# Kernel tuning notes

Measured on AMD Instinct MI355X. Metric: run time of the kernel, lower is better.

The kernel has to match this reference:

```python
import jax, jax.numpy as jnp
import numpy as np

N = 50000      # nodes
E = 800000     # edges (before self-loops)
D = 128        # hid_d
H = 8          # heads
C = D // H     # per-head channels
L = 3          # layers
SLOPE = 0.2    # GATv2 leaky_relu negative slope
EPS = 1e-5     # LayerNorm eps


def setup_inputs() -> dict:
    key = jax.random.key(0)
    ks = jax.random.split(key, 8)
    x = jax.random.normal(ks[0], (N, D), dtype=jnp.float32)
    ei = jax.random.randint(ks[1], (2, E), 0, N, dtype=jnp.int32)
    s = 1.0 / np.sqrt(D)
    Wl = jax.random.normal(ks[2], (L, D, D), dtype=jnp.float32) * s   # source transform per layer
    Wr = jax.random.normal(ks[3], (L, D, D), dtype=jnp.float32) * s   # target transform per layer
    att = jax.random.normal(ks[4], (L, H, C), dtype=jnp.float32) * (1.0 / np.sqrt(C))
    bias = jnp.zeros((L, D), dtype=jnp.float32)
    gamma = jnp.ones((L, D), dtype=jnp.float32)
    beta = jnp.zeros((L, D), dtype=jnp.float32)
    return {"x": x, "Wl": Wl, "Wr": Wr, "att": att, "bias": bias,
            "gamma": gamma, "beta": beta, "ei": ei}


def _layernorm(y, g, b):
    mu = jnp.mean(y, axis=-1, keepdims=True)
    var = jnp.mean(jnp.square(y - mu), axis=-1, keepdims=True)
    return (y - mu) * jax.lax.rsqrt(var + EPS) * g + b


def reference(x, Wl, Wr, att, bias, gamma, beta, ei):
    # append self-loops (PyG GATv2Conv default add_self_loops=True)
    loops = jnp.arange(N, dtype=ei.dtype)
    src = jnp.concatenate([ei[0], loops])  # [E+N]
    dst = jnp.concatenate([ei[1], loops])  # [E+N]
    h = x
    for l in range(L):
        xl = (h @ Wl[l]).reshape(N, H, C)   # source-side features
        xr = (h @ Wr[l]).reshape(N, H, C)   # target-side features
        feat = xl[src] + xr[dst]            # [E+N, H, C] per-edge gather
        logits = jnp.einsum('ehc,hc->eh', jax.nn.leaky_relu(feat, SLOPE), att[l])
        # segment softmax over incoming edges of each dst node
        m = jax.ops.segment_max(logits, dst, num_segments=N)
        ex = jnp.exp(logits - m[dst])
        denom = jax.ops.segment_sum(ex, dst, num_segments=N)
        alpha = ex / denom[dst]             # [E+N, H]
        msg = alpha[:, :, None] * xl[src]   # [E+N, H, C]
        out = jax.ops.segment_sum(msg, dst, num_segments=N).reshape(N, H * C) + bias[l]
        # wrapper: h = h + dropout(elu(norm(gat(h)))) ; dropout = identity (eval)
        h = h + jax.nn.elu(_layernorm(out, gamma[l], beta[l]))
    return h
```

## Files before the change

### kernel.cpp

```cpp
#include <hip/hip_runtime.h>
#include <hip/hip_fp16.h>
#include <math.h>

#define N_NODES 50000
#define N_EDGES 800000
#define D 128
#define L 3
#define SLOPE 0.2f
#define LN_EPS 1e-5f
#define ETOT (N_EDGES + N_NODES)
#define SCAN_BLOCKS ((N_NODES + 1023) / 1024)

typedef _Float16 half8 __attribute__((ext_vector_type(8)));
typedef _Float16 h4v  __attribute__((ext_vector_type(4)));
typedef _Float16 h2v  __attribute__((ext_vector_type(2)));
typedef float f32x4 __attribute__((ext_vector_type(4)));


__global__ void rank_hist_kernel(const int* __restrict__ ei, int* __restrict__ counts,
                                 int* __restrict__ rank) {
    int idx = blockIdx.x * blockDim.x + threadIdx.x;
    if (idx >= ETOT) return;
    int d = (idx < N_EDGES) ? ei[N_EDGES + idx] : (idx - N_EDGES);
    rank[idx] = atomicAdd(&counts[d], 1);
}

__global__ __launch_bounds__(1024) void scan1_kernel(const int* __restrict__ counts,
                                                     int* __restrict__ offsets,
                                                     int* __restrict__ bsum) {
    __shared__ int wsum[16];
    int tid = threadIdx.x;
    int lane = tid & 63, w = tid >> 6;
    int i = blockIdx.x * 1024 + tid;
    int v = (i < N_NODES) ? counts[i] : 0;
    int sc = v;
    #pragma unroll
    for (int off = 1; off < 64; off <<= 1) {
        int u = __shfl_up(sc, off);
        if (lane >= off) sc += u;
    }
    if (lane == 63) wsum[w] = sc;
    __syncthreads();
    if (w == 0) {
        int t2 = (lane < 16) ? wsum[lane] : 0;
        #pragma unroll
        for (int off = 1; off < 16; off <<= 1) {
            int u = __shfl_up(t2, off);
            if (lane >= off) t2 += u;
        }
        if (lane < 16) wsum[lane] = t2;
    }
    __syncthreads();
    int wpref = (w == 0) ? 0 : wsum[w - 1];
    if (i < N_NODES) offsets[i] = wpref + sc - v;
    if (tid == 0) bsum[blockIdx.x] = wsum[15];
}

__global__ __launch_bounds__(64) void scan2_kernel(const int* __restrict__ bsum,
                                                   int* __restrict__ bpre) {
    int lane = threadIdx.x;
    int v = (lane < SCAN_BLOCKS) ? bsum[lane] : 0;
    int sc = v;
    #pragma unroll
    for (int off = 1; off < 64; off <<= 1) {
        int u = __shfl_up(sc, off);
        if (lane >= off) sc += u;
    }
    if (lane < SCAN_BLOCKS) bpre[lane] = sc - v;
}

__global__ __launch_bounds__(1024) void scan3_kernel(int* __restrict__ offsets,
                                                     const int* __restrict__ bpre) {
    int i = blockIdx.x * 1024 + threadIdx.x;
    if (i < N_NODES) offsets[i] += bpre[blockIdx.x];
    if (i == 0) offsets[N_NODES] = ETOT;
}

__global__ void scatter_kernel(const int* __restrict__ ei, const int* __restrict__ offsets,
                               const int* __restrict__ rank,
                               unsigned short* __restrict__ sorted16) {
    int idx = blockIdx.x * blockDim.x + threadIdx.x;
    if (idx >= ETOT) return;
    int s, d;
    if (idx < N_EDGES) { s = ei[idx]; d = ei[N_EDGES + idx]; }
    else               { s = d = idx - N_EDGES; }
    sorted16[offsets[d] + rank[idx]] = (unsigned short)s;
}


__global__ __launch_bounds__(1024) void deg_hist_kernel(const int* __restrict__ counts,
                                                        int* __restrict__ blockhist) {
    __shared__ int lh[256];
    int tid = threadIdx.x;
    if (tid < 256) lh[tid] = 0;
    __syncthreads();
    int i = blockIdx.x * 1024 + tid;
    if (i < N_NODES) {
        int d = counts[i]; if (d > 255) d = 255;
        atomicAdd(&lh[d], 1);
    }
    __syncthreads();
    if (tid < 256) blockhist[blockIdx.x * 256 + tid] = lh[tid];
}

__global__ __launch_bounds__(256) void deg_scan_kernel(int* __restrict__ blockhist) {
    int d = threadIdx.x;
    int run = 0;
    #pragma unroll 1
    for (int b = 0; b < SCAN_BLOCKS; ++b) {
        int c = blockhist[b * 256 + d];
        blockhist[b * 256 + d] = run;
        run += c;
    }
    __shared__ int wsum[4];
    int lane = d & 63, w = d >> 6;
    int sc = run;
    #pragma unroll
    for (int off = 1; off < 64; off <<= 1) {
        int u = __shfl_up(sc, off);
        if (lane >= off) sc += u;
    }
    if (lane == 63) wsum[w] = sc;
    __syncthreads();
    int wpre = 0;
    #pragma unroll
    for (int k = 0; k < 4; ++k) wpre += (k < w) ? wsum[k] : 0;
    int binbase = wpre + sc - run;
    #pragma unroll 1
    for (int b = 0; b < SCAN_BLOCKS; ++b)
        blockhist[b * 256 + d] += binbase;
}

__global__ __launch_bounds__(1024) void deg_scatter_kernel(const int* __restrict__ counts,
                                                           const int* __restrict__ blockhist,
                                                           int* __restrict__ perm) {
    __shared__ int lh[256];
    int tid = threadIdx.x;
    if (tid < 256) lh[tid] = 0;
    __syncthreads();
    int i = blockIdx.x * 1024 + tid;
    if (i >= N_NODES) return;
    int d = counts[i]; if (d > 255) d = 255;
    int r = atomicAdd(&lh[d], 1);
    int pos = blockhist[blockIdx.x * 256 + d] + r;
    perm[pos] = i;
}


__global__ __launch_bounds__(256) void wfrag_kernel(const float* __restrict__ Wl,
                                                    const float* __restrict__ Wr,
                                                    _Float16* __restrict__ Wfrag) {
    int u = blockIdx.x * 256 + threadIdx.x;
    if (u >= 3 * 4096) return;
    int lane = u & 63, nt = (u >> 6) & 7, kt = (u >> 9) & 3, y = (u >> 11) & 1, l = u >> 12;
    int r = lane & 15, q = lane >> 4;
    const float* W = (y ? Wr : Wl) + (size_t)l * D * D;
    half8 v;
    #pragma unroll
    for (int j = 0; j < 8; ++j)
        v[j] = (_Float16)W[(kt * 32 + q * 8 + j) * D + nt * 16 + r];
    *(half8*)&Wfrag[(size_t)u * 8] = v;
}


template<bool AHALF>
__global__ __launch_bounds__(256) void gemm_mfma_kernel(
        const void* __restrict__ hsrc, const _Float16* __restrict__ WfragL,
        _Float16* __restrict__ xlh, _Float16* __restrict__ xrh) {
    __shared__ half8 Afrag[1024];
    int t = threadIdx.x;
    int row0 = blockIdx.x * 64;
    int w = t >> 6, lane = t & 63;
    int y = w >> 1, nh = w & 1;

    half8 bfrag[16];
    #pragma unroll
    for (int kt = 0; kt < 4; ++kt)
        #pragma unroll
        for (int n = 0; n < 4; ++n) {
            int nt = nh * 4 + n;
            bfrag[kt * 4 + n] =
                *(const half8*)&WfragL[(size_t)(((y * 4 + kt) * 8 + nt) * 64 + lane) * 8];
        }

    {
        int kt = t >> 6, q = (t >> 4) & 3, r = t & 15;
        int kc = kt * 4 + q;
        #pragma unroll
        for (int i = 0; i < 4; ++i) {
            int row = row0 + i * 16 + r;
            half8 v = {};
            if (row < N_NODES) {
                if constexpr (AHALF) {
                    const _Float16* h16 = (const _Float16*)hsrc;
                    v = *(const half8*)&h16[(size_t)row * D + kc * 8];
                } else {
                    const float* p = &((const float*)hsrc)[(size_t)row * D + kc * 8];
                    float4 f0 = *(const float4*)p;
                    float4 f1 = *(const float4*)(p + 4);
                    v[0] = (_Float16)f0.x; v[1] = (_Float16)f0.y;
                    v[2] = (_Float16)f0.z; v[3] = (_Float16)f0.w;
                    v[4] = (_Float16)f1.x; v[5] = (_Float16)f1.y;
                    v[6] = (_Float16)f1.z; v[7] = (_Float16)f1.w;
                }
            }
            Afrag[i * 256 + t] = v;
        }
    }
    __syncthreads();

    f32x4 acc[16];
    #pragma unroll
    for (int i = 0; i < 16; ++i) acc[i] = (f32x4){0.f, 0.f, 0.f, 0.f};
    #pragma unroll
    for (int mt = 0; mt < 4; ++mt) {
        #pragma unroll
        for (int kt = 0; kt < 4; ++kt) {
            half8 a = Afrag[mt * 256 + kt * 64 + lane];
            #pragma unroll
            for (int n = 0; n < 4; ++n)
                acc[mt * 4 + n] = __builtin_amdgcn_mfma_f32_16x16x32_f16(
                    a, bfrag[kt * 4 + n], acc[mt * 4 + n], 0, 0, 0);
        }
    }

    _Float16* out = y ? xrh : xlh;
    int rq = lane >> 4, rc = lane & 15;
    #pragma unroll
    for (int mt = 0; mt < 4; ++mt) {
        int rbase = row0 + mt * 16 + rq * 4;
        #pragma unroll
        for (int n = 0; n < 4; ++n) {
            int nt = nh * 4 + n;
            #pragma unroll
            for (int reg = 0; reg < 4; ++reg) {
                int row = rbase + reg;
                if (row < N_NODES)
                    out[(size_t)row * D + nt * 16 + rc] = (_Float16)acc[mt * 4 + n][reg];
            }
        }
    }
}


__device__ __forceinline__ float pair_reduce2(float p) {
    int t;
    t = __builtin_amdgcn_update_dpp(0, __float_as_int(p), 0xB1, 0xF, 0xF, true);
    p += __int_as_float(t);
    return p;
}

__device__ __forceinline__ float logit8(half8 v, half8 xr, const h2v* att4, h2v slope2) {
    float p = 0.f;
    #pragma unroll
    for (int i = 0; i < 4; ++i) {
        h2v a; a[0] = v[2 * i];  a[1] = v[2 * i + 1];
        h2v b; b[0] = xr[2 * i]; b[1] = xr[2 * i + 1];
        h2v f  = a + b;
        h2v lf = __builtin_elementwise_max(f, f * slope2);
        p = __builtin_amdgcn_fdot2(lf, att4[i], p, false);
    }
    return p;
}

template<int KUN, bool MASK>
__device__ __forceinline__ void edge_block(
        int j, int idx_bp, unsigned off, unsigned laneoff, const char* xlb,
        half8 xr8, const h2v* att4, h2v slope2, int cnt,
        float& s, float* acc) {
    half8 vs[KUN];
    #pragma unroll
    for (int k = 0; k < KUN; ++k) {
        int o = __builtin_amdgcn_ds_bpermute(idx_bp + 4 * (j + k), (int)off);
        vs[k] = *(const half8*)(xlb + ((unsigned)o + laneoff));
    }
    #pragma unroll
    for (int k = 0; k < KUN; ++k) {
        float p = logit8(vs[k], xr8, att4, slope2);
        p = pair_reduce2(p);
        float e = __builtin_amdgcn_exp2f(p);
        if (MASK) e = (j + k < cnt) ? e : 0.f;
        s += e;
        #pragma unroll
        for (int i = 0; i < 8; ++i)
            acc[i] = fmaf(e, (float)vs[k][i], acc[i]);
    }
}

__global__ __launch_bounds__(256) void gat_node_kernel(
        const _Float16* __restrict__ xlh, const _Float16* __restrict__ xrh,
        const int* __restrict__ offsets, const unsigned short* __restrict__ sorted16,
        const int* __restrict__ perm,
        const float* __restrict__ att_l, const float* __restrict__ bias_l,
        const float* __restrict__ gamma_l, const float* __restrict__ beta_l,
        const float* __restrict__ hin, float* __restrict__ hout,
        _Float16* __restrict__ h16out) {
    int wid = (blockIdx.x * blockDim.x + threadIdx.x) >> 6;
    if (wid * 4 >= N_NODES) return;
    int lane = threadIdx.x & 63;
    int g = lane >> 4, hl = lane & 15;
    int node = perm[wid * 4 + g];
    unsigned laneoff = hl * 16u;
    int idx_bp = g << 6;

    half8 xr8 = *(const half8*)&xrh[(size_t)node * D + hl * 8];
    float4 af0 = *(const float4*)&att_l[hl * 8];
    float4 af1 = *(const float4*)&att_l[hl * 8 + 4];
    h2v att4[4], slope2;
    att4[0][0] = (_Float16)(af0.x * 1.44269504f);
    att4[0][1] = (_Float16)(af0.y * 1.44269504f);
    att4[1][0] = (_Float16)(af0.z * 1.44269504f);
    att4[1][1] = (_Float16)(af0.w * 1.44269504f);
    att4[2][0] = (_Float16)(af1.x * 1.44269504f);
    att4[2][1] = (_Float16)(af1.y * 1.44269504f);
    att4[3][0] = (_Float16)(af1.z * 1.44269504f);
    att4[3][1] = (_Float16)(af1.w * 1.44269504f);
    slope2[0] = (_Float16)SLOPE;
    slope2[1] = (_Float16)SLOPE;

    int beg = offsets[node], end = offsets[node + 1];
    int deg = end - beg;
    int d0 = __builtin_amdgcn_readlane(deg, 0);
    int d1 = __builtin_amdgcn_readlane(deg, 16);
    int d2 = __builtin_amdgcn_readlane(deg, 32);
    int d3 = __builtin_amdgcn_readlane(deg, 48);
    int m01 = d0 > d1 ? d0 : d1, m23 = d2 > d3 ? d2 : d3;
    int degMax = m01 > m23 ? m01 : m23;
    int n01 = d0 < d1 ? d0 : d1, n23 = d2 < d3 ? d2 : d3;
    int degMin = n01 < n23 ? n01 : n23;

    float s = 0.f;
    float acc[8] = {0.f, 0.f, 0.f, 0.f, 0.f, 0.f, 0.f, 0.f};
    const char* xlb = (const char*)xlh;

    for (int c0 = 0; c0 < degMax; c0 += 16) {
        int rem = deg - c0;
        int cnt = rem > 16 ? 16 : rem;
        int cl  = cnt > 0 ? (hl < cnt ? hl : cnt - 1) : 0;
        int pos = cnt > 0 ? beg + c0 + cl : beg;
        unsigned off = ((unsigned)sorted16[pos]) << 8;
        int jmax = degMax - c0; if (jmax > 16) jmax = 16;
        int nfull = degMin - c0; if (nfull > 16) nfull = 16; if (nfull < 0) nfull = 0;
        int j = 0;
        for (; j + 8 <= nfull; j += 8)
            edge_block<8, false>(j, idx_bp, off, laneoff, xlb, xr8, att4, slope2,
                                 cnt, s, acc);
        for (; j + 4 <= nfull; j += 4)
            edge_block<4, false>(j, idx_bp, off, laneoff, xlb, xr8, att4, slope2,
                                 cnt, s, acc);
        for (; j + 4 <= jmax; j += 4)
            edge_block<4, true>(j, idx_bp, off, laneoff, xlb, xr8, att4, slope2,
                                cnt, s, acc);
        for (; j < jmax; ++j)
            edge_block<1, true>(j, idx_bp, off, laneoff, xlb, xr8, att4, slope2,
                                cnt, s, acc);
    }

    float inv = 1.f / s;
    float4 b0 = *(const float4*)&bias_l[hl * 8];
    float4 b1 = *(const float4*)&bias_l[hl * 8 + 4];
    float o[8];
    o[0] = acc[0] * inv + b0.x; o[1] = acc[1] * inv + b0.y;
    o[2] = acc[2] * inv + b0.z; o[3] = acc[3] * inv + b0.w;
    o[4] = acc[4] * inv + b1.x; o[5] = acc[5] * inv + b1.y;
    o[6] = acc[6] * inv + b1.z; o[7] = acc[7] * inv + b1.w;
    float sum = ((o[0] + o[1]) + (o[2] + o[3])) + ((o[4] + o[5]) + (o[6] + o[7]));
    float sq  = ((o[0] * o[0] + o[1] * o[1]) + (o[2] * o[2] + o[3] * o[3]))
              + ((o[4] * o[4] + o[5] * o[5]) + (o[6] * o[6] + o[7] * o[7]));
    #pragma unroll
    for (int msk = 1; msk < 16; msk <<= 1) {
        sum += __shfl_xor(sum, msk);
        sq  += __shfl_xor(sq, msk);
    }
    float mu   = sum * (1.f / 128.f);
    float var  = sq * (1.f / 128.f) - mu * mu;
    float rstd = rsqrtf(var + LN_EPS);
    float4 g0 = *(const float4*)&gamma_l[hl * 8];
    float4 g1 = *(const float4*)&gamma_l[hl * 8 + 4];
    float4 e0 = *(const float4*)&beta_l[hl * 8];
    float4 e1 = *(const float4*)&beta_l[hl * 8 + 4];
    float gam[8] = {g0.x, g0.y, g0.z, g0.w, g1.x, g1.y, g1.z, g1.w};
    float bet[8] = {e0.x, e0.y, e0.z, e0.w, e1.x, e1.y, e1.z, e1.w};
    size_t di = (size_t)node * D + hl * 8;
    float4 h0 = *(const float4*)&hin[di];
    float4 h1 = *(const float4*)&hin[di + 4];
    float hv[8] = {h0.x, h0.y, h0.z, h0.w, h1.x, h1.y, h1.z, h1.w};
    float y[8];
    #pragma unroll
    for (int i = 0; i < 8; ++i) {
        float t = (o[i] - mu) * rstd * gam[i] + bet[i];
        t = t > 0.f ? t : __expf(t) - 1.f;
        y[i] = hv[i] + t;
    }
    float4 w0 = make_float4(y[0], y[1], y[2], y[3]);
    float4 w1 = make_float4(y[4], y[5], y[6], y[7]);
    *(float4*)&hout[di]     = w0;
    *(float4*)&hout[di + 4] = w1;
    half8 h16v;
    #pragma unroll
    for (int i = 0; i < 8; ++i) h16v[i] = (_Float16)y[i];
    *(half8*)&h16out[di] = h16v;
}


extern "C" void kernel_launch(void* const* d_in, const int* in_sizes, int n_in,
                              void* d_out, int out_size, void* d_ws, size_t ws_size,
                              hipStream_t stream) {
    const float* x     = (const float*)d_in[0];
    const float* Wl    = (const float*)d_in[1];
    const float* Wr    = (const float*)d_in[2];
    const float* att   = (const float*)d_in[3];
    const float* bias  = (const float*)d_in[4];
    const float* gamma = (const float*)d_in[5];
    const float* beta  = (const float*)d_in[6];
    const int*   ei    = (const int*)d_in[7];
    float* h = (float*)d_out;

    char* ws = (char*)d_ws;
    _Float16* xlh = (_Float16*)ws;   ws += (size_t)N_NODES * D * sizeof(_Float16);
    _Float16* xrh = (_Float16*)ws;   ws += (size_t)N_NODES * D * sizeof(_Float16);
    _Float16* h16 = (_Float16*)ws;   ws += (size_t)N_NODES * D * sizeof(_Float16);
    _Float16* Wfrag = (_Float16*)ws; ws += (size_t)3 * 4096 * 8 * sizeof(_Float16);
    int* offsets = (int*)ws;         ws += (size_t)(N_NODES + 4) * sizeof(int);
    int* counts  = (int*)ws;         ws += (size_t)N_NODES * sizeof(int);
    int* bsum    = (int*)ws;         ws += 64 * sizeof(int);
    int* bpre    = (int*)ws;         ws += 64 * sizeof(int);
    int* blockhist = (int*)ws;       ws += (size_t)SCAN_BLOCKS * 256 * sizeof(int);
    int* perm    = (int*)ws;         ws += (size_t)N_NODES * sizeof(int);
    int* rank    = (int*)ws;         ws += (size_t)ETOT * sizeof(int);
    unsigned short* sorted16 = (unsigned short*)ws;

    wfrag_kernel<<<48, 256, 0, stream>>>(Wl, Wr, Wfrag);
    (void)hipMemsetAsync(counts, 0, (size_t)N_NODES * sizeof(int), stream);
    rank_hist_kernel<<<(ETOT + 255) / 256, 256, 0, stream>>>(ei, counts, rank);
    scan1_kernel<<<SCAN_BLOCKS, 1024, 0, stream>>>(counts, offsets, bsum);
    scan2_kernel<<<1, 64, 0, stream>>>(bsum, bpre);
    scan3_kernel<<<SCAN_BLOCKS, 1024, 0, stream>>>(offsets, bpre);
    scatter_kernel<<<(ETOT + 255) / 256, 256, 0, stream>>>(ei, offsets, rank, sorted16);
    deg_hist_kernel<<<SCAN_BLOCKS, 1024, 0, stream>>>(counts, blockhist);
    deg_scan_kernel<<<1, 256, 0, stream>>>(blockhist);
    deg_scatter_kernel<<<SCAN_BLOCKS, 1024, 0, stream>>>(counts, blockhist, perm);

    int gat_waves  = (N_NODES + 3) / 4;
    int gat_blocks = (gat_waves * 64 + 255) / 256;
    for (int l = 0; l < L; ++l) {
        const float* hin = (l == 0) ? x : h;
        if (l == 0)
            gemm_mfma_kernel<false><<<(N_NODES + 63) / 64, 256, 0, stream>>>(
                x, Wfrag + (size_t)l * 4096 * 8, xlh, xrh);
        else
            gemm_mfma_kernel<true><<<(N_NODES + 63) / 64, 256, 0, stream>>>(
                h16, Wfrag + (size_t)l * 4096 * 8, xlh, xrh);
        gat_node_kernel<<<gat_blocks, 256, 0, stream>>>(
            xlh, xrh, offsets, sorted16, perm,
            att + (size_t)l * D, bias + (size_t)l * D,
            gamma + (size_t)l * D, beta + (size_t)l * D, hin, h, h16);
    }
}
```

Before: 330.0 us.

## Fuse degree-sort kernels into scan kernels, transpose MFMA output, process high-degree nodes first

```diff
diff --git a/kernel.cpp b/kernel.cpp
--- a/kernel.cpp
+++ b/kernel.cpp
@@ -27,12 +27,20 @@
 
 __global__ __launch_bounds__(1024) void scan1_kernel(const int* __restrict__ counts,
                                                      int* __restrict__ offsets,
-                                                     int* __restrict__ bsum) {
+                                                     int* __restrict__ bsum,
+                                                     int* __restrict__ blockhist) {
     __shared__ int wsum[16];
+    __shared__ int lh[256];
     int tid = threadIdx.x;
+    if (tid < 256) lh[tid] = 0;
+    __syncthreads();
     int lane = tid & 63, w = tid >> 6;
     int i = blockIdx.x * 1024 + tid;
     int v = (i < N_NODES) ? counts[i] : 0;
+    if (i < N_NODES) {
+        int d = v; if (d > 255) d = 255;
+        atomicAdd(&lh[d], 1);
+    }
     int sc = v;
     #pragma unroll
     for (int off = 1; off < 64; off <<= 1) {
@@ -54,25 +62,68 @@
     int wpref = (w == 0) ? 0 : wsum[w - 1];
     if (i < N_NODES) offsets[i] = wpref + sc - v;
     if (tid == 0) bsum[blockIdx.x] = wsum[15];
-}
-
-__global__ __launch_bounds__(64) void scan2_kernel(const int* __restrict__ bsum,
-                                                   int* __restrict__ bpre) {
-    int lane = threadIdx.x;
-    int v = (lane < SCAN_BLOCKS) ? bsum[lane] : 0;
-    int sc = v;
+    __syncthreads();
+    if (tid < 256) blockhist[blockIdx.x * 256 + tid] = lh[tid];
+}
+
+__global__ __launch_bounds__(256) void scan2_kernel(const int* __restrict__ bsum,
+                                                    int* __restrict__ bpre,
+                                                    int* __restrict__ blockhist) {
+    int tid = threadIdx.x;
+    if (tid < 64) {
+        int lane = tid;
+        int v = (lane < SCAN_BLOCKS) ? bsum[lane] : 0;
+        int sc = v;
+        #pragma unroll
+        for (int off = 1; off < 64; off <<= 1) {
+            int u = __shfl_up(sc, off);
+            if (lane >= off) sc += u;
+        }
+        if (lane < SCAN_BLOCKS) bpre[lane] = sc - v;
+    }
+    int d = tid;
+    int run = 0;
+    #pragma unroll 1
+    for (int b = 0; b < SCAN_BLOCKS; ++b) {
+        int c = blockhist[b * 256 + d];
+        blockhist[b * 256 + d] = run;
+        run += c;
+    }
+    __shared__ int wsum[4];
+    int lane = d & 63, w = d >> 6;
+    int sc = run;
     #pragma unroll
     for (int off = 1; off < 64; off <<= 1) {
         int u = __shfl_up(sc, off);
         if (lane >= off) sc += u;
     }
-    if (lane < SCAN_BLOCKS) bpre[lane] = sc - v;
+    if (lane == 63) wsum[w] = sc;
+    __syncthreads();
+    int wpre = 0;
+    #pragma unroll
+    for (int k = 0; k < 4; ++k) wpre += (k < w) ? wsum[k] : 0;
+    int binbase = wpre + sc - run;
+    #pragma unroll 1
+    for (int b = 0; b < SCAN_BLOCKS; ++b)
+        blockhist[b * 256 + d] += binbase;
 }
 
 __global__ __launch_bounds__(1024) void scan3_kernel(int* __restrict__ offsets,
-                                                     const int* __restrict__ bpre) {
-    int i = blockIdx.x * 1024 + threadIdx.x;
-    if (i < N_NODES) offsets[i] += bpre[blockIdx.x];
+                                                     const int* __restrict__ bpre,
+                                                     const int* __restrict__ counts,
+                                                     const int* __restrict__ blockhist,
+                                                     int* __restrict__ perm) {
+    __shared__ int lh[256];
+    int tid = threadIdx.x;
+    if (tid < 256) lh[tid] = 0;
+    __syncthreads();
+    int i = blockIdx.x * 1024 + tid;
+    if (i < N_NODES) {
+        offsets[i] += bpre[blockIdx.x];
+        int d = counts[i]; if (d > 255) d = 255;
+        int r = atomicAdd(&lh[d], 1);
+        perm[blockhist[blockIdx.x * 256 + d] + r] = i;
+    }
     if (i == 0) offsets[N_NODES] = ETOT;
 }
 
@@ -88,65 +139,6 @@
 }
 
 
-__global__ __launch_bounds__(1024) void deg_hist_kernel(const int* __restrict__ counts,
-                                                        int* __restrict__ blockhist) {
-    __shared__ int lh[256];
-    int tid = threadIdx.x;
-    if (tid < 256) lh[tid] = 0;
-    __syncthreads();
-    int i = blockIdx.x * 1024 + tid;
-    if (i < N_NODES) {
-        int d = counts[i]; if (d > 255) d = 255;
-        atomicAdd(&lh[d], 1);
-    }
-    __syncthreads();
-    if (tid < 256) blockhist[blockIdx.x * 256 + tid] = lh[tid];
-}
-
-__global__ __launch_bounds__(256) void deg_scan_kernel(int* __restrict__ blockhist) {
-    int d = threadIdx.x;
-    int run = 0;
-    #pragma unroll 1
-    for (int b = 0; b < SCAN_BLOCKS; ++b) {
-        int c = blockhist[b * 256 + d];
-        blockhist[b * 256 + d] = run;
-        run += c;
-    }
-    __shared__ int wsum[4];
-    int lane = d & 63, w = d >> 6;
-    int sc = run;
-    #pragma unroll
-    for (int off = 1; off < 64; off <<= 1) {
-        int u = __shfl_up(sc, off);
-        if (lane >= off) sc += u;
-    }
-    if (lane == 63) wsum[w] = sc;
-    __syncthreads();
-    int wpre = 0;
-    #pragma unroll
-    for (int k = 0; k < 4; ++k) wpre += (k < w) ? wsum[k] : 0;
-    int binbase = wpre + sc - run;
-    #pragma unroll 1
-    for (int b = 0; b < SCAN_BLOCKS; ++b)
-        blockhist[b * 256 + d] += binbase;
-}
-
-__global__ __launch_bounds__(1024) void deg_scatter_kernel(const int* __restrict__ counts,
-                                                           const int* __restrict__ blockhist,
-                                                           int* __restrict__ perm) {
-    __shared__ int lh[256];
-    int tid = threadIdx.x;
-    if (tid < 256) lh[tid] = 0;
-    __syncthreads();
-    int i = blockIdx.x * 1024 + tid;
-    if (i >= N_NODES) return;
-    int d = counts[i]; if (d > 255) d = 255;
-    int r = atomicAdd(&lh[d], 1);
-    int pos = blockhist[blockIdx.x * 256 + d] + r;
-    perm[pos] = i;
-}
-
-
 __global__ __launch_bounds__(256) void wfrag_kernel(const float* __restrict__ Wl,
                                                     const float* __restrict__ Wr,
                                                     _Float16* __restrict__ Wfrag) {
@@ -177,9 +169,9 @@
     #pragma unroll
     for (int kt = 0; kt < 4; ++kt)
         #pragma unroll
-        for (int n = 0; n < 4; ++n) {
-            int nt = nh * 4 + n;
-            bfrag[kt * 4 + n] =
+        for (int f = 0; f < 4; ++f) {
+            int nt = nh * 4 + f;
+            bfrag[kt * 4 + f] =
                 *(const half8*)&WfragL[(size_t)(((y * 4 + kt) * 8 + nt) * 64 + lane) * 8];
         }
 
@@ -213,30 +205,32 @@
     #pragma unroll
     for (int i = 0; i < 16; ++i) acc[i] = (f32x4){0.f, 0.f, 0.f, 0.f};
     #pragma unroll
-    for (int mt = 0; mt < 4; ++mt) {
+    for (int ntile = 0; ntile < 4; ++ntile) {
         #pragma unroll
         for (int kt = 0; kt < 4; ++kt) {
-            half8 a = Afrag[mt * 256 + kt * 64 + lane];
+            half8 a = Afrag[ntile * 256 + kt * 64 + lane];
             #pragma unroll
-            for (int n = 0; n < 4; ++n)
-                acc[mt * 4 + n] = __builtin_amdgcn_mfma_f32_16x16x32_f16(
-                    a, bfrag[kt * 4 + n], acc[mt * 4 + n], 0, 0, 0);
+            for (int f = 0; f < 4; ++f)
+                acc[f * 4 + ntile] = __builtin_amdgcn_mfma_f32_16x16x32_f16(
+                    bfrag[kt * 4 + f], a, acc[f * 4 + ntile], 0, 0, 0);
         }
     }
 
     _Float16* out = y ? xrh : xlh;
-    int rq = lane >> 4, rc = lane & 15;
-    #pragma unroll
-    for (int mt = 0; mt < 4; ++mt) {
-        int rbase = row0 + mt * 16 + rq * 4;
-        #pragma unroll
-        for (int n = 0; n < 4; ++n) {
-            int nt = nh * 4 + n;
+    int nr = lane & 15, fq = lane >> 4;
+    #pragma unroll
+    for (int ntile = 0; ntile < 4; ++ntile) {
+        int row = row0 + ntile * 16 + nr;
+        if (row < N_NODES) {
             #pragma unroll
-            for (int reg = 0; reg < 4; ++reg) {
-                int row = rbase + reg;
-                if (row < N_NODES)
-                    out[(size_t)row * D + nt * 16 + rc] = (_Float16)acc[mt * 4 + n][reg];
+            for (int f = 0; f < 4; ++f) {
+                int fb = nh * 64 + f * 16 + fq * 4;
+                h4v v4;
+                v4[0] = (_Float16)acc[f * 4 + ntile][0];
+                v4[1] = (_Float16)acc[f * 4 + ntile][1];
+                v4[2] = (_Float16)acc[f * 4 + ntile][2];
+                v4[3] = (_Float16)acc[f * 4 + ntile][3];
+                *(h4v*)&out[(size_t)row * D + fb] = v4;
             }
         }
     }
@@ -299,7 +293,7 @@
     if (wid * 4 >= N_NODES) return;
     int lane = threadIdx.x & 63;
     int g = lane >> 4, hl = lane & 15;
-    int node = perm[wid * 4 + g];
+    int node = perm[N_NODES - 4 - wid * 4 + g];
     unsigned laneoff = hl * 16u;
     int idx_bp = g << 6;
 
@@ -433,13 +427,10 @@
     wfrag_kernel<<<48, 256, 0, stream>>>(Wl, Wr, Wfrag);
     (void)hipMemsetAsync(counts, 0, (size_t)N_NODES * sizeof(int), stream);
     rank_hist_kernel<<<(ETOT + 255) / 256, 256, 0, stream>>>(ei, counts, rank);
-    scan1_kernel<<<SCAN_BLOCKS, 1024, 0, stream>>>(counts, offsets, bsum);
-    scan2_kernel<<<1, 64, 0, stream>>>(bsum, bpre);
-    scan3_kernel<<<SCAN_BLOCKS, 1024, 0, stream>>>(offsets, bpre);
+    scan1_kernel<<<SCAN_BLOCKS, 1024, 0, stream>>>(counts, offsets, bsum, blockhist);
+    scan2_kernel<<<1, 256, 0, stream>>>(bsum, bpre, blockhist);
+    scan3_kernel<<<SCAN_BLOCKS, 1024, 0, stream>>>(offsets, bpre, counts, blockhist, perm);
     scatter_kernel<<<(ETOT + 255) / 256, 256, 0, stream>>>(ei, offsets, rank, sorted16);
-    deg_hist_kernel<<<SCAN_BLOCKS, 1024, 0, stream>>>(counts, blockhist);
-    deg_scan_kernel<<<1, 256, 0, stream>>>(blockhist);
-    deg_scatter_kernel<<<SCAN_BLOCKS, 1024, 0, stream>>>(counts, blockhist, perm);
 
     int gat_waves  = (N_NODES + 3) / 4;
     int gat_blocks = (gat_waves * 64 + 255) / 256;
```

Measured after the change: 327.4 us. No clear change (-0.8%).
